# Kernel optimization log

Measured on AMD Instinct MI355X. Metric: run time of the kernel, lower is better.

## Reference

```python
import jax, jax.numpy as jnp
import numpy as np

EPS = 1e-9


def setup_inputs() -> dict:
    key = jax.random.key(0)
    k1, k2, k3, k4 = jax.random.split(key, 4)
    B, D, U = 1024, 512, 512
    x = jax.random.normal(k1, (B, D), dtype=jnp.float32)
    w = jax.random.normal(k2, (D, U), dtype=jnp.float32)
    p = jax.random.normal(k3, (D, U), dtype=jnp.float32)
    b = jax.random.normal(k4, (U,), dtype=jnp.float32)
    return {"x": x, "w": w, "p": p, "b": b}


def reference(x, w, p, b):
    # x: [B, D]; w, p: [D, U]; b: [U]
    xe = x[..., None] + EPS                      # [B, D, 1]
    abs_pow = jnp.abs(xe) ** p                   # [B, D, U]
    is_neg = xe < 0                              # [B, D, 1]
    odd_mask = jnp.mod(p, 2) != 0                # [D, U]
    signed = jnp.where(odd_mask & is_neg, -abs_pow, abs_pow)
    z = jnp.sum(w * signed, axis=1) + b          # [B, U]
    return z  # linear activation
```

## Files before the change

kernel.cpp:

```cpp
#include <hip/hip_runtime.h>
#include <math.h>

#define EPS 1e-9f

constexpr int Bn = 1024, Dn = 512, Un = 512;
constexpr int BM = 32;
constexpr int BU = 64;
constexpr int DK = 16;
constexpr int SPLITD = 8;
constexpr int DPB = Dn / SPLITD;
constexpr int NCHUNK = DPB / DK;

typedef float v4f __attribute__((ext_vector_type(4)));

__device__ __forceinline__ int swz(int d) { return ((d >> 2) & 3) << 3; }

template <bool USE_WS>
__global__ __launch_bounds__(256, 4) void power_layer(
    const float* __restrict__ x, const float* __restrict__ w,
    const float* __restrict__ p, const float* __restrict__ bias,
    float* __restrict__ outp)
{
    __shared__ float sL[DK][BM];
    __shared__ float sP[DK][BU];
    __shared__ float sW[DK][BU];
    __shared__ float sWX[DK][BU];

    const int tid = threadIdx.x;
    const int tx  = tid & 15;
    const int ty  = tid >> 4;
    const int tx4 = tx * 4;
    const int ty2 = ty * 2;
    const int ub = blockIdx.x * BU;
    const int bb = blockIdx.y * BM;
    const int d0 = blockIdx.z * DPB;

    v4f acc[2] = {};

    for (int ch = 0; ch < NCHUNK; ++ch) {
        const int db = d0 + ch * DK;

        if (tid < 128) {
            const int r  = tid >> 2;
            const int dq = (tid & 3) << 2;
            const float4 xv = *reinterpret_cast<const float4*>(
                &x[(size_t)(bb + r) * Dn + db + dq]);
            const float* xs = reinterpret_cast<const float*>(&xv);
            #pragma unroll
            for (int j = 0; j < 4; ++j) {
                const float xe = xs[j] + EPS;
                const float La = __builtin_amdgcn_logf(fabsf(xe)) + 64.0f;
                const int dd = dq + j;
                sL[dd][r ^ swz(dd)] = (xe < 0.0f) ? -La : La;
            }
        }
        {
            const int d  = tid >> 4;
            const int uq = (tid & 15) << 2;
            const size_t gi = (size_t)(db + d) * Un + ub + uq;
            const float4 pv = *reinterpret_cast<const float4*>(&p[gi]);
            const float4 wv = *reinterpret_cast<const float4*>(&w[gi]);
            const float* ps  = reinterpret_cast<const float*>(&pv);
            const float* wsv = reinterpret_cast<const float*>(&wv);
            float4 wxv;
            float* wxs = reinterpret_cast<float*>(&wxv);
            #pragma unroll
            for (int j = 0; j < 4; ++j) {
                const bool odd = (fmodf(ps[j], 2.0f) != 0.0f);
                wxs[j] = odd ? -wsv[j] : wsv[j];
            }
            *reinterpret_cast<float4*>(&sP[d][uq])  = pv;
            *reinterpret_cast<float4*>(&sW[d][uq])  = wv;
            *reinterpret_cast<float4*>(&sWX[d][uq]) = wxv;
        }
        __syncthreads();

        #pragma unroll 4
        for (int d = 0; d < DK; ++d) {
            const float2 Lv = *reinterpret_cast<const float2*>(&sL[d][ty2 ^ swz(d)]);
            const v4f    Pv = *reinterpret_cast<const v4f*>(&sP[d][tx4]);
            const float* Ls = reinterpret_cast<const float*>(&Lv);

            #pragma unroll
            for (int r = 0; r < 2; ++r) {
                const float Ld = fabsf(Ls[r]) - 64.0f;
                const bool  ng = Ls[r] < 0.0f;
                const v4f Wsel = *reinterpret_cast<const v4f*>(
                    ng ? &sWX[d][tx4] : &sW[d][tx4]);

                const v4f t = Pv * Ld;
                v4f e;
                #pragma unroll
                for (int c = 0; c < 4; ++c)
                    e[c] = __builtin_amdgcn_exp2f(t[c]);
                acc[r] = __builtin_elementwise_fma(Wsel, e, acc[r]);
            }
        }
        __syncthreads();
    }

    if (USE_WS) {
        float* dst = outp + ((size_t)blockIdx.z * Bn + bb + ty2) * Un + ub + tx4;
        #pragma unroll
        for (int r = 0; r < 2; ++r)
            *reinterpret_cast<v4f*>(dst + (size_t)r * Un) = acc[r];
    } else {
        if (blockIdx.z == 0) {
            const v4f bv = *reinterpret_cast<const v4f*>(&bias[ub + tx4]);
            #pragma unroll
            for (int r = 0; r < 2; ++r)
                acc[r] += bv;
        }
        #pragma unroll
        for (int r = 0; r < 2; ++r) {
            const int row = bb + ty2 + r;
            #pragma unroll
            for (int c = 0; c < 4; ++c)
                atomicAdd(&outp[(size_t)row * Un + ub + tx4 + c], acc[r][c]);
        }
    }
}

__global__ __launch_bounds__(256) void reduce_ws(
    const float* __restrict__ ws, const float* __restrict__ bias,
    float* __restrict__ out)
{
    const int nf4 = (Bn * Un) / 4;
    const int i = blockIdx.x * 256 + threadIdx.x;
    if (i >= nf4) return;
    const v4f* w4 = reinterpret_cast<const v4f*>(ws);
    v4f a = w4[i];
    #pragma unroll
    for (int z = 1; z < SPLITD; ++z)
        a += w4[(size_t)z * nf4 + i];
    a += reinterpret_cast<const v4f*>(bias)[i & (Un / 4 - 1)];
    reinterpret_cast<v4f*>(out)[i] = a;
}

extern "C" void kernel_launch(void* const* d_in, const int* in_sizes, int n_in,
                              void* d_out, int out_size, void* d_ws, size_t ws_size,
                              hipStream_t stream) {
    const float* x = (const float*)d_in[0];
    const float* w = (const float*)d_in[1];
    const float* p = (const float*)d_in[2];
    const float* b = (const float*)d_in[3];
    float* out = (float*)d_out;

    const dim3 grid(Un / BU, Bn / BM, SPLITD);
    const size_t need = (size_t)SPLITD * Bn * Un * sizeof(float);

    if (ws_size >= need) {
        float* wsf = (float*)d_ws;
        power_layer<true><<<grid, dim3(256), 0, stream>>>(x, w, p, b, wsf);
        reduce_ws<<<dim3((Bn * Un / 4 + 255) / 256), dim3(256), 0, stream>>>(wsf, b, out);
    } else {
        hipMemsetAsync(out, 0, (size_t)out_size * sizeof(float), stream);
        power_layer<false><<<grid, dim3(256), 0, stream>>>(x, w, p, b, out);
    }
}
```

Before: 108.5 us.

## Prefetch next chunk's x, p, w into registers during compute

Global loads for the next D-chunk are issued into registers right after the shared-memory stores, so their latency overlaps the exp2/FMA inner loop of the current chunk. The log and sign-flip preprocessing now runs on register-held values before a barrier, and the shared-memory writes move after it. This hides global-load latency at the cost of extra registers per thread and an extra barrier per chunk, which may cut occupancy under the 4-blocks launch bound.

```diff
diff --git a/kernel.cpp b/kernel.cpp
--- a/kernel.cpp
+++ b/kernel.cpp
@@ -35,45 +35,66 @@
     const int bb = blockIdx.y * BM;
     const int d0 = blockIdx.z * DPB;
 
+    const int xr  = tid >> 2;
+    const int xdq = (tid & 3) << 2;
+    const int pd  = tid >> 4;
+    const int puq = (tid & 15) << 2;
+
+    float4 xv = {}, pv = {}, wv = {};
+    if (tid < 128)
+        xv = *reinterpret_cast<const float4*>(&x[(size_t)(bb + xr) * Dn + d0 + xdq]);
+    {
+        const size_t gi = (size_t)(d0 + pd) * Un + ub + puq;
+        pv = *reinterpret_cast<const float4*>(&p[gi]);
+        wv = *reinterpret_cast<const float4*>(&w[gi]);
+    }
+
     v4f acc[2] = {};
 
     for (int ch = 0; ch < NCHUNK; ++ch) {
-        const int db = d0 + ch * DK;
-
+        float Lenc[4];
         if (tid < 128) {
-            const int r  = tid >> 2;
-            const int dq = (tid & 3) << 2;
-            const float4 xv = *reinterpret_cast<const float4*>(
-                &x[(size_t)(bb + r) * Dn + db + dq]);
             const float* xs = reinterpret_cast<const float*>(&xv);
             #pragma unroll
             for (int j = 0; j < 4; ++j) {
                 const float xe = xs[j] + EPS;
                 const float La = __builtin_amdgcn_logf(fabsf(xe)) + 64.0f;
-                const int dd = dq + j;
-                sL[dd][r ^ swz(dd)] = (xe < 0.0f) ? -La : La;
+                Lenc[j] = (xe < 0.0f) ? -La : La;
             }
         }
+        float4 wxv;
         {
-            const int d  = tid >> 4;
-            const int uq = (tid & 15) << 2;
-            const size_t gi = (size_t)(db + d) * Un + ub + uq;
-            const float4 pv = *reinterpret_cast<const float4*>(&p[gi]);
-            const float4 wv = *reinterpret_cast<const float4*>(&w[gi]);
             const float* ps  = reinterpret_cast<const float*>(&pv);
             const float* wsv = reinterpret_cast<const float*>(&wv);
-            float4 wxv;
             float* wxs = reinterpret_cast<float*>(&wxv);
             #pragma unroll
             for (int j = 0; j < 4; ++j) {
                 const bool odd = (fmodf(ps[j], 2.0f) != 0.0f);
                 wxs[j] = odd ? -wsv[j] : wsv[j];
             }
-            *reinterpret_cast<float4*>(&sP[d][uq])  = pv;
-            *reinterpret_cast<float4*>(&sW[d][uq])  = wv;
-            *reinterpret_cast<float4*>(&sWX[d][uq]) = wxv;
         }
+
         __syncthreads();
+        if (tid < 128) {
+            #pragma unroll
+            for (int j = 0; j < 4; ++j) {
+                const int dd = xdq + j;
+                sL[dd][xr ^ swz(dd)] = Lenc[j];
+            }
+        }
+        *reinterpret_cast<float4*>(&sP[pd][puq])  = pv;
+        *reinterpret_cast<float4*>(&sW[pd][puq])  = wv;
+        *reinterpret_cast<float4*>(&sWX[pd][puq]) = wxv;
+        __syncthreads();
+
+        if (ch + 1 < NCHUNK) {
+            const int db = d0 + (ch + 1) * DK;
+            if (tid < 128)
+                xv = *reinterpret_cast<const float4*>(&x[(size_t)(bb + xr) * Dn + db + xdq]);
+            const size_t gi = (size_t)(db + pd) * Un + ub + puq;
+            pv = *reinterpret_cast<const float4*>(&p[gi]);
+            wv = *reinterpret_cast<const float4*>(&w[gi]);
+        }
 
         #pragma unroll 4
         for (int d = 0; d < DK; ++d) {
```

Measured after the change: 109.5 us. Within noise of the previous version (+0.9%).
